# Optimization experiments

Hardware: AMD Instinct MI355X
Metric: run time of the kernel (lower is better)

## Reference

```python
import jax, jax.numpy as jnp
import numpy as np

NITERS = 5  # mean-field iterations (niters in __init__)


def setup_inputs() -> dict:
    key = jax.random.key(0)
    k1, k2 = jax.random.split(key)
    B, L, C, H, W = 2, 21, 3, 96, 96
    E0 = jax.random.normal(k1, (B, L, H, W), dtype=jnp.float32)
    Refs = jax.random.normal(k2, (B, C, H, W), dtype=jnp.float32)
    # potts_init: weight = ones(L,L) - eye(L)
    Mu_W = jnp.ones((L, L), dtype=jnp.float32) - jnp.eye(L, dtype=jnp.float32)
    return {"E0": E0, "Refs": Refs, "Mu_W": Mu_W}


def _affinity(Refs):
    # Reference-guided dense adjacency (BatchedAdjacency): row-normalized
    # Gaussian affinity on guide features, one N x N matrix per batch element.
    B, C, H, W = Refs.shape
    N = H * W
    f = Refs.reshape(B, C, N).transpose(0, 2, 1)  # [B, N, C]
    sq = jnp.sum(f * f, axis=-1)  # [B, N]
    D = sq[:, :, None] + sq[:, None, :] - 2.0 * jnp.einsum('bnc,bmc->bnm', f, f)
    A = jnp.exp(-0.5 * D)  # [B, N, N]
    return A / jnp.sum(A, axis=-1, keepdims=True)


def reference(E0, Refs, Mu_W):
    B, L, H, W = E0.shape
    N = H * W
    A = _affinity(Refs)  # computed once, reused every iteration
    E0f = E0.reshape(B, L, N)
    Qf = jax.nn.softmax(-E0f, axis=1)  # Q = softmax(-E0, dim=1)
    for _ in range(NITERS):
        # Potts compatibility transform (channel mixing): Mu(Q)
        M = jnp.einsum('kl,bln->bkn', Mu_W, Qf)
        # adjacency message passing: W(Mu(Q), Refs)
        msg = jnp.einsum('bnm,blm->bln', A, M)
        Qf = jax.nn.softmax(-(E0f + msg), axis=1)
    return Qf.reshape(B, L, H, W)
```

## Files before the change

### kernel.cpp

```cpp
#include <hip/hip_runtime.h>
#include <hip/hip_bf16.h>


#define BB 2
#define LL 21
#define LP (LL + 1)
#define NNPX 9216
#define NITERS 5
#define LOG2E 1.4426950408889634f

#define BARRIER() asm volatile("s_waitcnt lgkmcnt(0)\n\ts_barrier" ::: "memory")

typedef __attribute__((ext_vector_type(8))) short short8;
typedef __attribute__((ext_vector_type(4))) float f32x4;
typedef __attribute__((ext_vector_type(4))) unsigned int u32x4;

static __device__ inline unsigned int pk_bf16(float a, float b) {
    __hip_bfloat162 h = __float22bfloat162_rn(make_float2(a, b));
    unsigned int u;
    __builtin_memcpy(&u, &h, 4);
    return u;
}

__global__ __launch_bounds__(256) void k_prep(
        const float* __restrict__ E0, const float* __restrict__ Refs,
        const float* __restrict__ Mu,
        float4* __restrict__ FN, float4* __restrict__ FS,
        __hip_bfloat16* __restrict__ MQ) {
    __shared__ float muS[LL * LL];
    __shared__ float red1[4][64], red2[4][64];
    __shared__ float Qs[LL][64];

    int t = threadIdx.x;
    for (int i = t; i < LL * LL; i += 256) muS[i] = Mu[i];

    int q = t >> 6, px = t & 63;
    int pid = blockIdx.x * 64 + px;
    int b = pid / NNPX, n = pid % NNPX;

    if (q == 0) {
        const float* rb = Refs + (size_t)b * 3 * NNPX + n;
        float r0 = rb[0], r1 = rb[NNPX], r2 = rb[2 * NNPX];
        FN[pid] = make_float4(r0, r1, r2, 0.f);
        float g = -0.5f * (r0 * r0 + r1 * r1 + r2 * r2);
        FS[pid] = make_float4(g * LOG2E, r0 * LOG2E, r1 * LOG2E, r2 * LOG2E);
    }

    int l0 = q * 6;
    const float* eb = E0 + (size_t)b * LL * NNPX + n;
    float x[6];
    float mx = -1e30f;
    #pragma unroll
    for (int i = 0; i < 6; ++i) {
        int l = l0 + i;
        x[i] = (l < LL) ? -eb[(size_t)l * NNPX] : -1e30f;
        mx = fmaxf(mx, x[i]);
    }
    red1[q][px] = mx;
    __syncthreads();
    mx = fmaxf(fmaxf(red1[0][px], red1[1][px]), fmaxf(red1[2][px], red1[3][px]));
    float s = 0.f;
    #pragma unroll
    for (int i = 0; i < 6; ++i) { x[i] = __builtin_amdgcn_exp2f((x[i] - mx) * LOG2E); s += x[i]; }
    red2[q][px] = s;
    __syncthreads();
    float rs = __builtin_amdgcn_rcpf(red2[0][px] + red2[1][px] + red2[2][px] + red2[3][px]);
    #pragma unroll
    for (int i = 0; i < 6; ++i) if (l0 + i < LL) Qs[l0 + i][px] = x[i] * rs;
    __syncthreads();

    __hip_bfloat16* mq = MQ + (size_t)b * LL * NNPX + n;
    #pragma unroll
    for (int j = 0; j < 6; ++j) {
        int k = l0 + j;
        if (k < LL) {
            float a = 0.f;
            for (int l = 0; l < LL; ++l) a += muS[k * LL + l] * Qs[l][px];
            mq[(size_t)k * NNPX] = __float2bfloat16(a);
        }
    }
}

__global__ __launch_bounds__(256, 8) void k_accum(
        const float4* __restrict__ FS, const float4* __restrict__ FN,
        const unsigned int* __restrict__ MQbf, float* __restrict__ Ppart, int S) {
    __shared__ __align__(16) float FSlds[2][256];
    __shared__ __align__(16) unsigned short Mlds[2][32 * 64];

    int t = threadIdx.x;
    int rb = blockIdx.x;
    int s  = blockIdx.y;
    int b  = rb / 144;
    int n0 = (rb % 144) * 64;
    int wv = t >> 6, lane = t & 63;
    int lr = lane & 15, g = lane >> 4;

    for (int i = t; i < 11 * 32 * 2; i += 256) {
        int bufi = i >= 11 * 32;
        int ii = i - bufi * 11 * 32;
        int r = 21 + (ii >> 5), d = ii & 31;
        ((unsigned int*)&Mlds[bufi][r * 64])[d] = (r == 21) ? 0x3F803F80u : 0u;
    }

    int row = wv * 16 + lr;
    float4 fv = FN[b * NNPX + n0 + row];
    float fnx = fv.x, fny = fv.y, fnz = fv.z;

    const int T  = 144 / S;
    const int t0 = s * T;
    const float* fs32 = (const float*)(FS + (size_t)b * NNPX);
    const unsigned int* mqb = MQbf + (size_t)b * LL * (NNPX / 2);

    int mloc = t >> 2, comp = t & 3;
    int fslot = (mloc & ~7) | ((mloc ^ (mloc >> 3)) & 7);
    int fsw = fslot * 4 + comp;

    int sl0 = t >> 5, sm0 = t & 31;
    int sl1 = (t + 256) >> 5, sm1 = (t + 256) & 31;
    int sl2 = (t + 512) >> 5, sm2 = (t + 512) & 31;
    int mw0 = sl0 * 32 + (((sm0 >> 2) ^ (sl0 & 7)) << 2) + (sm0 & 3);
    int mw1 = sl1 * 32 + (((sm1 >> 2) ^ (sl1 & 7)) << 2) + (sm1 & 3);
    int mw2 = sl2 * 32 + (((sm2 >> 2) ^ (sl2 & 7)) << 2) + (sm2 & 3);

    int ib0 = lr * 64 + ((g ^ (lr & 7)) << 3);
    int ib1 = lr * 64 + (((g + 4) ^ (lr & 7)) << 3);
    int ib2 = (16 + lr) * 64 + ((g ^ (lr & 7)) << 3);
    int ib3 = (16 + lr) * 64 + (((g + 4) ^ (lr & 7)) << 3);

    f32x4 acc0 = {0.f, 0.f, 0.f, 0.f};
    f32x4 acc1 = {0.f, 0.f, 0.f, 0.f};

    int g8 = g * 8;

    float fsr;
    unsigned int mrA0, mrA1, mrA2;

    auto LOAD = [&](int tile) {
        int m0 = (t0 + tile) * 64;
        fsr = fs32[m0 * 4 + t];
        int mo0 = (t0 + tile) * 32;
        mrA0 = mqb[(size_t)sl0 * (NNPX / 2) + mo0 + sm0];
        mrA1 = mqb[(size_t)sl1 * (NNPX / 2) + mo0 + sm1];
        if (t < 160) mrA2 = mqb[(size_t)sl2 * (NNPX / 2) + mo0 + sm2];
    };
    auto STORE = [&](int buf) {
        FSlds[buf][fsw] = fsr;
        ((unsigned int*)Mlds[buf])[mw0] = mrA0;
        ((unsigned int*)Mlds[buf])[mw1] = mrA1;
        if (t < 160) ((unsigned int*)Mlds[buf])[mw2] = mrA2;
    };
    auto COMPUTE = [&](int buf) {
        const float4* FB = (const float4*)FSlds[buf];
        float w[8];
        #pragma unroll
        for (int j = 0; j < 8; ++j) {
            float4 F = FB[g8 + (j ^ g)];
            w[j] = __builtin_amdgcn_exp2f(F.x + fnx * F.y + fny * F.z + fnz * F.w);
        }
        u32x4 ap;
        #pragma unroll
        for (int j = 0; j < 4; ++j) ap[j] = pk_bf16(w[2 * j], w[2 * j + 1]);
        short8 a0 = __builtin_bit_cast(short8, ap);
        #pragma unroll
        for (int j = 0; j < 8; ++j) {
            float4 F = FB[32 + g8 + ((j ^ g) ^ 4)];
            w[j] = __builtin_amdgcn_exp2f(F.x + fnx * F.y + fny * F.z + fnz * F.w);
        }
        #pragma unroll
        for (int j = 0; j < 4; ++j) ap[j] = pk_bf16(w[2 * j], w[2 * j + 1]);
        short8 a1 = __builtin_bit_cast(short8, ap);

        short8 b00 = *(const short8*)&Mlds[buf][ib0];
        short8 b01 = *(const short8*)&Mlds[buf][ib1];
        short8 b10 = *(const short8*)&Mlds[buf][ib2];
        short8 b11 = *(const short8*)&Mlds[buf][ib3];
        acc0 = __builtin_amdgcn_mfma_f32_16x16x32_bf16(a0, b00, acc0, 0, 0, 0);
        acc0 = __builtin_amdgcn_mfma_f32_16x16x32_bf16(a1, b01, acc0, 0, 0, 0);
        acc1 = __builtin_amdgcn_mfma_f32_16x16x32_bf16(a0, b10, acc1, 0, 0, 0);
        acc1 = __builtin_amdgcn_mfma_f32_16x16x32_bf16(a1, b11, acc1, 0, 0, 0);
    };

    LOAD(0);
    STORE(0);
    BARRIER();

    for (int tt = 0; tt < T; ++tt) {
        int cur = tt & 1;
        if (tt + 1 < T) LOAD(tt + 1);
        COMPUTE(cur);
        if (tt + 1 < T) STORE(cur ^ 1);
        BARRIER();
    }

    int col = lane & 15, qr = lane >> 4;
    float* pp = Ppart + ((size_t)(s * BB + b) * LP) * NNPX;
    for (int r = 0; r < 4; ++r) {
        int n = n0 + wv * 16 + qr * 4 + r;
        pp[(size_t)col * NNPX + n] = acc0[r];
        if (col < LP - 16) pp[(size_t)(16 + col) * NNPX + n] = acc1[r];
    }
}

template <bool LAST>
__global__ __launch_bounds__(256) void k_softmax(
        const float* __restrict__ E0, const float* __restrict__ Ppart,
        const float* __restrict__ Mu,
        __hip_bfloat16* __restrict__ MQ, float* __restrict__ Out, int S) {
    __shared__ float muS[LL * LL];
    __shared__ float rsumS[64];
    __shared__ float red1[4][64], red2[4][64];
    __shared__ float Qs[LL][64];

    int t = threadIdx.x;
    if (!LAST) for (int i = t; i < LL * LL; i += 256) muS[i] = Mu[i];

    int q = t >> 6, px = t & 63;
    int pid = blockIdx.x * 64 + px;
    int b = pid / NNPX, n = pid % NNPX;

    int l0 = q * 6;
    const float* ppb = Ppart + n;
    const float* eb = E0 + (size_t)b * LL * NNPX + n;

    float Pa[6], e0v[6];
    #pragma unroll
    for (int i = 0; i < 6; ++i) {
        int l = l0 + i;
        Pa[i] = 0.f; e0v[i] = 0.f;
        if (l < LL) {
            for (int s = 0; s < S; ++s)
                Pa[i] += ppb[((size_t)(s * BB + b) * LP + l) * NNPX];
            e0v[i] = eb[(size_t)l * NNPX];
        }
    }
    if (q == 3) {
        float racc = 0.f;
        for (int s = 0; s < S; ++s)
            racc += ppb[((size_t)(s * BB + b) * LP + LL) * NNPX];
        rsumS[px] = racc;
    }
    __syncthreads();
    float rinv = __builtin_amdgcn_rcpf(rsumS[px]);

    float x[6];
    float mx = -1e30f;
    #pragma unroll
    for (int i = 0; i < 6; ++i) {
        x[i] = (l0 + i < LL) ? -(e0v[i] + Pa[i] * rinv) : -1e30f;
        mx = fmaxf(mx, x[i]);
    }
    red1[q][px] = mx;
    __syncthreads();
    mx = fmaxf(fmaxf(red1[0][px], red1[1][px]), fmaxf(red1[2][px], red1[3][px]));
    float ssum = 0.f;
    #pragma unroll
    for (int i = 0; i < 6; ++i) { x[i] = __builtin_amdgcn_exp2f((x[i] - mx) * LOG2E); ssum += x[i]; }
    red2[q][px] = ssum;
    __syncthreads();
    float rs = __builtin_amdgcn_rcpf(red2[0][px] + red2[1][px] + red2[2][px] + red2[3][px]);

    if (LAST) {
        float* ob = Out + (size_t)b * LL * NNPX + n;
        #pragma unroll
        for (int i = 0; i < 6; ++i) if (l0 + i < LL) ob[(size_t)(l0 + i) * NNPX] = x[i] * rs;
    } else {
        #pragma unroll
        for (int i = 0; i < 6; ++i) if (l0 + i < LL) Qs[l0 + i][px] = x[i] * rs;
        __syncthreads();
        __hip_bfloat16* mq = MQ + (size_t)b * LL * NNPX + n;
        #pragma unroll
        for (int j = 0; j < 6; ++j) {
            int k = l0 + j;
            if (k < LL) {
                float a = 0.f;
                for (int l = 0; l < LL; ++l) a += muS[k * LL + l] * Qs[l][px];
                mq[(size_t)k * NNPX] = __float2bfloat16(a);
            }
        }
    }
}

extern "C" void kernel_launch(void* const* d_in, const int* in_sizes, int n_in,
                              void* d_out, int out_size, void* d_ws, size_t ws_size,
                              hipStream_t stream) {
    const float* E0   = (const float*)d_in[0];
    const float* Refs = (const float*)d_in[1];
    const float* Mu   = (const float*)d_in[2];
    float* out = (float*)d_out;

    char* w = (char*)d_ws;
    size_t off = 0;
    auto alloc = [&](size_t bytes) {
        void* p = w + off;
        off += (bytes + 255) & ~(size_t)255;
        return p;
    };
    float4* FN     = (float4*)alloc((size_t)BB * NNPX * sizeof(float4));
    float4* FS     = (float4*)alloc((size_t)BB * NNPX * sizeof(float4));
    __hip_bfloat16* MQbf = (__hip_bfloat16*)alloc((size_t)BB * LL * NNPX * sizeof(__hip_bfloat16));

    size_t per = (size_t)BB * LP * NNPX * sizeof(float);
    size_t avail = ws_size > off ? ws_size - off : 0;
    int Smax = (int)(avail / (per + 256));
    static const int divs[] = {8, 6, 4, 3, 2, 1};
    int S = 1;
    for (int i = 0; i < 6; ++i) if (divs[i] <= Smax) { S = divs[i]; break; }
    float* Ppart = (float*)alloc((size_t)S * per);

    k_prep<<<BB * NNPX / 64, 256, 0, stream>>>(E0, Refs, Mu, FN, FS, MQbf);
    for (int it = 0; it < NITERS; ++it) {
        k_accum<<<dim3(288, S), 256, 0, stream>>>(FS, FN, (const unsigned int*)MQbf, Ppart, S);
        if (it == NITERS - 1)
            k_softmax<true><<<BB * NNPX / 64, 256, 0, stream>>>(E0, Ppart, Mu, MQbf, out, S);
        else
            k_softmax<false><<<BB * NNPX / 64, 256, 0, stream>>>(E0, Ppart, Mu, MQbf, out, S);
    }
}
```

Before: 390.8 us.

## Fuse all iterations into one cooperative persistent kernel with grid syncs

Replaces the prep kernel and the per-iteration accumulate and softmax launches with a single cooperative kernel over 864 blocks. Grid-wide syncs separate the stages, and a multi-launch path is kept as a fallback if the cooperative launch fails. The split factor is fixed at 3 instead of being chosen from workspace size. The FN buffer is dropped, and pixel features are recovered from FS by rescaling. This aims to remove launch gaps between the 11 kernels, at the cost of grid barriers, idle blocks during the softmax stages (only a third of blocks work there), and lower occupancy from the launch bounds of 4 blocks.

```diff
diff --git a/kernel.cpp b/kernel.cpp
--- a/kernel.cpp
+++ b/kernel.cpp
@@ -1,5 +1,8 @@
 #include <hip/hip_runtime.h>
 #include <hip/hip_bf16.h>
+#include <hip/hip_cooperative_groups.h>
+
+namespace cg = cooperative_groups;
 
 
 #define BB 2
@@ -7,7 +10,10 @@
 #define LP (LL + 1)
 #define NNPX 9216
 #define NITERS 5
+#define SSPLIT 3
+#define TT (144 / SSPLIT)
 #define LOG2E 1.4426950408889634f
+#define INVL2E 0.6931471805599453f
 
 #define BARRIER() asm volatile("s_waitcnt lgkmcnt(0)\n\ts_barrier" ::: "memory")
 
@@ -22,26 +28,24 @@
     return u;
 }
 
-__global__ __launch_bounds__(256) void k_prep(
+static __device__ void prep_body(
+        int rb, int t,
         const float* __restrict__ E0, const float* __restrict__ Refs,
         const float* __restrict__ Mu,
-        float4* __restrict__ FN, float4* __restrict__ FS,
-        __hip_bfloat16* __restrict__ MQ) {
-    __shared__ float muS[LL * LL];
-    __shared__ float red1[4][64], red2[4][64];
-    __shared__ float Qs[LL][64];
-
-    int t = threadIdx.x;
-    for (int i = t; i < LL * LL; i += 256) muS[i] = Mu[i];
+        float4* __restrict__ FS, __hip_bfloat16* __restrict__ MQ) {
+    __shared__ float muS_p[LL * LL];
+    __shared__ float red1_p[4][64], red2_p[4][64];
+    __shared__ float Qs_p[LL][64];
+
+    for (int i = t; i < LL * LL; i += 256) muS_p[i] = Mu[i];
 
     int q = t >> 6, px = t & 63;
-    int pid = blockIdx.x * 64 + px;
+    int pid = rb * 64 + px;
     int b = pid / NNPX, n = pid % NNPX;
 
     if (q == 0) {
-        const float* rb = Refs + (size_t)b * 3 * NNPX + n;
-        float r0 = rb[0], r1 = rb[NNPX], r2 = rb[2 * NNPX];
-        FN[pid] = make_float4(r0, r1, r2, 0.f);
+        const float* rbp = Refs + (size_t)b * 3 * NNPX + n;
+        float r0 = rbp[0], r1 = rbp[NNPX], r2 = rbp[2 * NNPX];
         float g = -0.5f * (r0 * r0 + r1 * r1 + r2 * r2);
         FS[pid] = make_float4(g * LOG2E, r0 * LOG2E, r1 * LOG2E, r2 * LOG2E);
     }
@@ -56,17 +60,17 @@
         x[i] = (l < LL) ? -eb[(size_t)l * NNPX] : -1e30f;
         mx = fmaxf(mx, x[i]);
     }
-    red1[q][px] = mx;
-    __syncthreads();
-    mx = fmaxf(fmaxf(red1[0][px], red1[1][px]), fmaxf(red1[2][px], red1[3][px]));
+    red1_p[q][px] = mx;
+    __syncthreads();
+    mx = fmaxf(fmaxf(red1_p[0][px], red1_p[1][px]), fmaxf(red1_p[2][px], red1_p[3][px]));
     float s = 0.f;
     #pragma unroll
     for (int i = 0; i < 6; ++i) { x[i] = __builtin_amdgcn_exp2f((x[i] - mx) * LOG2E); s += x[i]; }
-    red2[q][px] = s;
-    __syncthreads();
-    float rs = __builtin_amdgcn_rcpf(red2[0][px] + red2[1][px] + red2[2][px] + red2[3][px]);
-    #pragma unroll
-    for (int i = 0; i < 6; ++i) if (l0 + i < LL) Qs[l0 + i][px] = x[i] * rs;
+    red2_p[q][px] = s;
+    __syncthreads();
+    float rs = __builtin_amdgcn_rcpf(red2_p[0][px] + red2_p[1][px] + red2_p[2][px] + red2_p[3][px]);
+    #pragma unroll
+    for (int i = 0; i < 6; ++i) if (l0 + i < LL) Qs_p[l0 + i][px] = x[i] * rs;
     __syncthreads();
 
     __hip_bfloat16* mq = MQ + (size_t)b * LL * NNPX + n;
@@ -75,21 +79,19 @@
         int k = l0 + j;
         if (k < LL) {
             float a = 0.f;
-            for (int l = 0; l < LL; ++l) a += muS[k * LL + l] * Qs[l][px];
+            for (int l = 0; l < LL; ++l) a += muS_p[k * LL + l] * Qs_p[l][px];
             mq[(size_t)k * NNPX] = __float2bfloat16(a);
         }
     }
 }
 
-__global__ __launch_bounds__(256, 8) void k_accum(
-        const float4* __restrict__ FS, const float4* __restrict__ FN,
-        const unsigned int* __restrict__ MQbf, float* __restrict__ Ppart, int S) {
+static __device__ void accum_body(
+        int rb, int s, int t,
+        const float4* __restrict__ FS, const unsigned int* __restrict__ MQbf,
+        float* __restrict__ Ppart) {
     __shared__ __align__(16) float FSlds[2][256];
     __shared__ __align__(16) unsigned short Mlds[2][32 * 64];
 
-    int t = threadIdx.x;
-    int rb = blockIdx.x;
-    int s  = blockIdx.y;
     int b  = rb / 144;
     int n0 = (rb % 144) * 64;
     int wv = t >> 6, lane = t & 63;
@@ -103,11 +105,10 @@
     }
 
     int row = wv * 16 + lr;
-    float4 fv = FN[b * NNPX + n0 + row];
-    float fnx = fv.x, fny = fv.y, fnz = fv.z;
-
-    const int T  = 144 / S;
-    const int t0 = s * T;
+    float4 fv = FS[(size_t)b * NNPX + n0 + row];
+    float fnx = fv.y * INVL2E, fny = fv.z * INVL2E, fnz = fv.w * INVL2E;
+
+    const int t0 = s * TT;
     const float* fs32 = (const float*)(FS + (size_t)b * NNPX);
     const unsigned int* mqb = MQbf + (size_t)b * LL * (NNPX / 2);
 
@@ -152,12 +153,12 @@
     auto COMPUTE = [&](int buf) {
         const float4* FB = (const float4*)FSlds[buf];
         float w[8];
+        u32x4 ap;
         #pragma unroll
         for (int j = 0; j < 8; ++j) {
             float4 F = FB[g8 + (j ^ g)];
             w[j] = __builtin_amdgcn_exp2f(F.x + fnx * F.y + fny * F.z + fnz * F.w);
         }
-        u32x4 ap;
         #pragma unroll
         for (int j = 0; j < 4; ++j) ap[j] = pk_bf16(w[2 * j], w[2 * j + 1]);
         short8 a0 = __builtin_bit_cast(short8, ap);
@@ -184,11 +185,11 @@
     STORE(0);
     BARRIER();
 
-    for (int tt = 0; tt < T; ++tt) {
+    for (int tt = 0; tt < TT; ++tt) {
         int cur = tt & 1;
-        if (tt + 1 < T) LOAD(tt + 1);
+        if (tt + 1 < TT) LOAD(tt + 1);
         COMPUTE(cur);
-        if (tt + 1 < T) STORE(cur ^ 1);
+        if (tt + 1 < TT) STORE(cur ^ 1);
         BARRIER();
     }
 
@@ -201,21 +202,20 @@
     }
 }
 
-template <bool LAST>
-__global__ __launch_bounds__(256) void k_softmax(
+static __device__ void softmax_body(
+        int rb, int t, bool last,
         const float* __restrict__ E0, const float* __restrict__ Ppart,
         const float* __restrict__ Mu,
-        __hip_bfloat16* __restrict__ MQ, float* __restrict__ Out, int S) {
-    __shared__ float muS[LL * LL];
-    __shared__ float rsumS[64];
-    __shared__ float red1[4][64], red2[4][64];
-    __shared__ float Qs[LL][64];
-
-    int t = threadIdx.x;
-    if (!LAST) for (int i = t; i < LL * LL; i += 256) muS[i] = Mu[i];
+        __hip_bfloat16* __restrict__ MQ, float* __restrict__ Out) {
+    __shared__ float muS_s[LL * LL];
+    __shared__ float rsumS_s[64];
+    __shared__ float red1_s[4][64], red2_s[4][64];
+    __shared__ float Qs_s[LL][64];
+
+    if (!last) for (int i = t; i < LL * LL; i += 256) muS_s[i] = Mu[i];
 
     int q = t >> 6, px = t & 63;
-    int pid = blockIdx.x * 64 + px;
+    int pid = rb * 64 + px;
     int b = pid / NNPX, n = pid % NNPX;
 
     int l0 = q * 6;
@@ -228,19 +228,19 @@
         int l = l0 + i;
         Pa[i] = 0.f; e0v[i] = 0.f;
         if (l < LL) {
-            for (int s = 0; s < S; ++s)
+            for (int s = 0; s < SSPLIT; ++s)
                 Pa[i] += ppb[((size_t)(s * BB + b) * LP + l) * NNPX];
             e0v[i] = eb[(size_t)l * NNPX];
         }
     }
     if (q == 3) {
         float racc = 0.f;
-        for (int s = 0; s < S; ++s)
+        for (int s = 0; s < SSPLIT; ++s)
             racc += ppb[((size_t)(s * BB + b) * LP + LL) * NNPX];
-        rsumS[px] = racc;
-    }
-    __syncthreads();
-    float rinv = __builtin_amdgcn_rcpf(rsumS[px]);
+        rsumS_s[px] = racc;
+    }
+    __syncthreads();
+    float rinv = __builtin_amdgcn_rcpf(rsumS_s[px]);
 
     float x[6];
     float mx = -1e30f;
@@ -249,23 +249,23 @@
         x[i] = (l0 + i < LL) ? -(e0v[i] + Pa[i] * rinv) : -1e30f;
         mx = fmaxf(mx, x[i]);
     }
-    red1[q][px] = mx;
-    __syncthreads();
-    mx = fmaxf(fmaxf(red1[0][px], red1[1][px]), fmaxf(red1[2][px], red1[3][px]));
+    red1_s[q][px] = mx;
+    __syncthreads();
+    mx = fmaxf(fmaxf(red1_s[0][px], red1_s[1][px]), fmaxf(red1_s[2][px], red1_s[3][px]));
     float ssum = 0.f;
     #pragma unroll
     for (int i = 0; i < 6; ++i) { x[i] = __builtin_amdgcn_exp2f((x[i] - mx) * LOG2E); ssum += x[i]; }
-    red2[q][px] = ssum;
-    __syncthreads();
-    float rs = __builtin_amdgcn_rcpf(red2[0][px] + red2[1][px] + red2[2][px] + red2[3][px]);
-
-    if (LAST) {
+    red2_s[q][px] = ssum;
+    __syncthreads();
+    float rs = __builtin_amdgcn_rcpf(red2_s[0][px] + red2_s[1][px] + red2_s[2][px] + red2_s[3][px]);
+
+    if (last) {
         float* ob = Out + (size_t)b * LL * NNPX + n;
         #pragma unroll
         for (int i = 0; i < 6; ++i) if (l0 + i < LL) ob[(size_t)(l0 + i) * NNPX] = x[i] * rs;
     } else {
         #pragma unroll
-        for (int i = 0; i < 6; ++i) if (l0 + i < LL) Qs[l0 + i][px] = x[i] * rs;
+        for (int i = 0; i < 6; ++i) if (l0 + i < LL) Qs_s[l0 + i][px] = x[i] * rs;
         __syncthreads();
         __hip_bfloat16* mq = MQ + (size_t)b * LL * NNPX + n;
         #pragma unroll
@@ -273,11 +273,46 @@
             int k = l0 + j;
             if (k < LL) {
                 float a = 0.f;
-                for (int l = 0; l < LL; ++l) a += muS[k * LL + l] * Qs[l][px];
+                for (int l = 0; l < LL; ++l) a += muS_s[k * LL + l] * Qs_s[l][px];
                 mq[(size_t)k * NNPX] = __float2bfloat16(a);
             }
         }
     }
+}
+
+__global__ __launch_bounds__(256, 4) void k_fused(
+        const float* E0, const float* Refs, const float* Mu,
+        float4* FS, __hip_bfloat16* MQ, float* Ppart, float* Out) {
+    cg::grid_group grid = cg::this_grid();
+    int t = threadIdx.x;
+    int bx = blockIdx.x;
+    int rb = bx % 288;
+    int s  = bx / 288;
+
+    if (s == 0) prep_body(rb, t, E0, Refs, Mu, FS, MQ);
+    grid.sync();
+
+    for (int it = 0; it < NITERS; ++it) {
+        accum_body(rb, s, t, FS, (const unsigned int*)MQ, Ppart);
+        grid.sync();
+        if (s == 0) softmax_body(rb, t, it == NITERS - 1, E0, Ppart, Mu, MQ, Out);
+        grid.sync();
+    }
+}
+
+__global__ __launch_bounds__(256) void k_prep_w(
+        const float* E0, const float* Refs, const float* Mu,
+        float4* FS, __hip_bfloat16* MQ) {
+    prep_body(blockIdx.x, threadIdx.x, E0, Refs, Mu, FS, MQ);
+}
+__global__ __launch_bounds__(256, 4) void k_accum_w(
+        const float4* FS, const unsigned int* MQbf, float* Ppart) {
+    accum_body(blockIdx.x % 288, blockIdx.x / 288, threadIdx.x, FS, MQbf, Ppart);
+}
+__global__ __launch_bounds__(256) void k_softmax_w(
+        const float* E0, const float* Ppart, const float* Mu,
+        __hip_bfloat16* MQ, float* Out, int last) {
+    softmax_body(blockIdx.x, threadIdx.x, last != 0, E0, Ppart, Mu, MQ, Out);
 }
 
 extern "C" void kernel_launch(void* const* d_in, const int* in_sizes, int n_in,
@@ -295,24 +330,21 @@
         off += (bytes + 255) & ~(size_t)255;
         return p;
     };
-    float4* FN     = (float4*)alloc((size_t)BB * NNPX * sizeof(float4));
-    float4* FS     = (float4*)alloc((size_t)BB * NNPX * sizeof(float4));
+    float4* FS = (float4*)alloc((size_t)BB * NNPX * sizeof(float4));
     __hip_bfloat16* MQbf = (__hip_bfloat16*)alloc((size_t)BB * LL * NNPX * sizeof(__hip_bfloat16));
-
-    size_t per = (size_t)BB * LP * NNPX * sizeof(float);
-    size_t avail = ws_size > off ? ws_size - off : 0;
-    int Smax = (int)(avail / (per + 256));
-    static const int divs[] = {8, 6, 4, 3, 2, 1};
-    int S = 1;
-    for (int i = 0; i < 6; ++i) if (divs[i] <= Smax) { S = divs[i]; break; }
-    float* Ppart = (float*)alloc((size_t)S * per);
-
-    k_prep<<<BB * NNPX / 64, 256, 0, stream>>>(E0, Refs, Mu, FN, FS, MQbf);
-    for (int it = 0; it < NITERS; ++it) {
-        k_accum<<<dim3(288, S), 256, 0, stream>>>(FS, FN, (const unsigned int*)MQbf, Ppart, S);
-        if (it == NITERS - 1)
-            k_softmax<true><<<BB * NNPX / 64, 256, 0, stream>>>(E0, Ppart, Mu, MQbf, out, S);
-        else
-            k_softmax<false><<<BB * NNPX / 64, 256, 0, stream>>>(E0, Ppart, Mu, MQbf, out, S);
-    }
-}
+    float* Ppart = (float*)alloc((size_t)SSPLIT * BB * LP * NNPX * sizeof(float));
+
+    void* args[] = {(void*)&E0, (void*)&Refs, (void*)&Mu,
+                    (void*)&FS, (void*)&MQbf, (void*)&Ppart, (void*)&out};
+    hipError_t err = hipLaunchCooperativeKernel(
+        (const void*)k_fused, dim3(288 * SSPLIT), dim3(256), args, 0, stream);
+
+    if (err != hipSuccess) {
+        k_prep_w<<<BB * NNPX / 64, 256, 0, stream>>>(E0, Refs, Mu, FS, MQbf);
+        for (int it = 0; it < NITERS; ++it) {
+            k_accum_w<<<288 * SSPLIT, 256, 0, stream>>>(FS, (const unsigned int*)MQbf, Ppart);
+            k_softmax_w<<<BB * NNPX / 64, 256, 0, stream>>>(
+                E0, Ppart, Mu, MQbf, out, it == NITERS - 1 ? 1 : 0);
+        }
+    }
+}
```

Result: slower. 1.429 ms (+265.6%).
